# Optimization experiments

Measured on AMD Instinct MI355X. Metric: run time of the kernel, lower is better.

Reference implementation:

```python
import jax, jax.numpy as jnp
import numpy as np

D_IN, D_K, D_V = 768, 128, 768


def setup_inputs() -> dict:
    key = jax.random.key(0)
    ks = jax.random.split(key, 7)
    x = jax.random.normal(ks[0], (4, 2048, D_IN), dtype=jnp.float32)
    s_in = 1.0 / np.sqrt(D_IN)
    Wq = jax.random.uniform(ks[1], (D_IN, D_K), minval=-s_in, maxval=s_in, dtype=jnp.float32)
    bq = jax.random.uniform(ks[2], (D_K,), minval=-s_in, maxval=s_in, dtype=jnp.float32)
    Wk = jax.random.uniform(ks[3], (D_IN, D_K), minval=-s_in, maxval=s_in, dtype=jnp.float32)
    bk = jax.random.uniform(ks[4], (D_K,), minval=-s_in, maxval=s_in, dtype=jnp.float32)
    Wv = jax.random.uniform(ks[5], (D_IN, D_V), minval=-s_in, maxval=s_in, dtype=jnp.float32)
    bv = jax.random.uniform(ks[6], (D_V,), minval=-s_in, maxval=s_in, dtype=jnp.float32)
    return {"x": x, "Wq": Wq, "bq": bq, "Wk": Wk, "bk": bk, "Wv": Wv, "bv": bv}


def reference(x, Wq, bq, Wk, bk, Wv, bv):
    # q,k: [b,t,d_k]; v: [b,t,d_v]
    q = jnp.einsum('bti,ik->btk', x, Wq) + bq
    k = jnp.einsum('bti,ik->btk', x, Wk) + bk
    v = jnp.einsum('bti,iv->btv', x, Wv) + bv
    scale = 1.0 / jnp.sqrt(jnp.asarray(D_K, dtype=jnp.float32))
    scores = jnp.einsum('bqk,btk->bqt', q, k) * scale  # [b,t,t]
    attn = jax.nn.softmax(scores, axis=-1)
    return jnp.einsum('bqt,btv->bqv', attn, v)
```

## Files before the change

### kernel.cpp

```cpp
#include <hip/hip_runtime.h>
#include <stdint.h>

typedef unsigned short u16;
typedef __attribute__((ext_vector_type(8))) short short8;
typedef __attribute__((ext_vector_type(4))) float f32x4;

#define BATCH 4
#define SEQ   2048
#define DIN   768
#define DK    128
#define DV    768
#define MTOT  (BATCH*SEQ)
#define NQKV  1024

__device__ __forceinline__ u16 f2bf(float f) {
  union { float f; uint32_t u; } v; v.f = f;
  uint32_t r = v.u + 0x7FFFu + ((v.u >> 16) & 1u);
  return (u16)(r >> 16);
}
__device__ __forceinline__ float bf2f(u16 h) {
  union { uint32_t u; float f; } v; v.u = ((uint32_t)h) << 16;
  return v.f;
}

__global__ __launch_bounds__(256) void pack_all(
    const float* __restrict__ Wq, const float* __restrict__ bq,
    const float* __restrict__ Wk, const float* __restrict__ bk,
    const float* __restrict__ Wv, const float* __restrict__ bv,
    u16* __restrict__ WbT, float* __restrict__ biasP) {
  const float qs = 0.088388347648318447f;
  __shared__ u16 tile[64][72];
  int y = blockIdx.y;
  const float* W; u16* dst; int ldw, nb; float sc;
  if (y < 2)      { W = Wq; dst = WbT;                       ldw = DK; sc = qs;   nb = y;     }
  else if (y < 4) { W = Wk; dst = WbT + (size_t)DK * DIN;    ldw = DK; sc = 1.0f; nb = y - 2; }
  else            { W = Wv; dst = WbT + (size_t)2*DK * DIN;  ldw = DV; sc = 1.0f; nb = y - 4; }
  int i0 = blockIdx.x * 64;
  int n0 = nb * 64;
  int tid = threadIdx.x;
  if (blockIdx.x == 0 && y == 0) {
    for (int n = tid; n < NQKV; n += 256)
      biasP[n] = (n < DK) ? bq[n] * qs : (n < 2*DK ? bk[n - DK] : bv[n - 2*DK]);
  }
  int tr = tid >> 2;
  int tc = (tid & 3) * 16;
  const float* src = W + (size_t)(i0 + tr) * ldw + n0 + tc;
  u16 o[16];
#pragma unroll
  for (int u = 0; u < 16; u += 4) {
    float4 v = *(const float4*)(src + u);
    o[u] = f2bf(v.x * sc); o[u+1] = f2bf(v.y * sc); o[u+2] = f2bf(v.z * sc); o[u+3] = f2bf(v.w * sc);
  }
  *(uint4*)&tile[tr][tc]     = *(const uint4*)&o[0];
  *(uint4*)&tile[tr][tc + 8] = *(const uint4*)&o[8];
  __syncthreads();
  u16 tmp[16];
#pragma unroll
  for (int u = 0; u < 16; ++u) tmp[u] = tile[tc + u][tr];
  u16* d = dst + (size_t)(n0 + tr) * DIN + i0 + tc;
  *(uint4*)d       = *(const uint4*)&tmp[0];
  *(uint4*)(d + 8) = *(const uint4*)&tmp[8];
}

__global__ void convert_x(const float* __restrict__ x, u16* __restrict__ xb) {
  int i = (blockIdx.x * blockDim.x + threadIdx.x) * 4;
  float4 v = *(const float4*)(x + i);
  u16 o[4] = { f2bf(v.x), f2bf(v.y), f2bf(v.z), f2bf(v.w) };
  *(uint2*)(xb + i) = *(const uint2*)o;
}

template<int MODE, int NJ>
__global__ __launch_bounds__(512, 4) void gemm_nt(
    const u16* __restrict__ A, int lda, long long sA,
    const u16* __restrict__ BT, int ldb, long long sB,
    void* __restrict__ C0, void* __restrict__ C1, int ldc, long long sC,
    int K, int gx, int gy, const float* __restrict__ bias)
{
  __shared__ u16 As[2][128][64];
  __shared__ u16 Bs[2][NJ * 64][64];
  const int tid = threadIdx.x;
  const int l   = tid & 63;
  const int wid = tid >> 6;
  const int wm  = wid >> 2;
  const int wn  = wid & 3;

  const int nwg = gridDim.x;
  const int cpx = nwg >> 3;
  const int bid = blockIdx.x;
  const int wg  = (bid & 7) * cpx + (bid >> 3);
  const int z   = wg / (gx * gy);
  const int rem = wg - z * gx * gy;
  const int by  = rem / gx;
  const int bx  = rem - by * gx;
  const int m0  = bx * 128;
  const int n0  = by * (NJ * 64);

  A  += (size_t)z * (size_t)sA;
  BT += (size_t)z * (size_t)sB;

  f32x4 acc[4][NJ] = {};
  f32x4 accO[4] = {};
  const short8 kOnes = {16256,16256,16256,16256,16256,16256,16256,16256};

  const int lr = l >> 3;
  const int lc = ((l & 7) ^ lr) * 8;

  const int CH = 2 + NJ;
  const int ca = wid * CH;
  auto STAGE = [&](int buf, int k0) {
#pragma unroll
    for (int i = 0; i < CH; ++i) {
      int c = ca + i;
      if (c < 16) {
        const u16* src = A + (size_t)(m0 + c * 8 + lr) * lda + k0 + lc;
        __builtin_amdgcn_global_load_lds(
            (const __attribute__((address_space(1))) unsigned int*)src,
            (__attribute__((address_space(3))) unsigned int*)&As[buf][c * 8][0],
            16, 0, 0);
      } else {
        int cb = c - 16;
        const u16* src = BT + (size_t)(n0 + cb * 8 + lr) * ldb + k0 + lc;
        __builtin_amdgcn_global_load_lds(
            (const __attribute__((address_space(1))) unsigned int*)src,
            (__attribute__((address_space(3))) unsigned int*)&Bs[buf][cb * 8][0],
            16, 0, 0);
      }
    }
  };

  STAGE(0, 0);
  __syncthreads();

  int cur = 0;
  for (int k0 = 0; k0 < K; k0 += 64) {
    if (k0 + 64 < K) STAGE(cur ^ 1, k0 + 64);
#pragma unroll
    for (int ks = 0; ks < 2; ++ks) {
      short8 af[4], bg[NJ];
#pragma unroll
      for (int i = 0; i < 4; ++i) {
        int row  = wm * 64 + i * 16 + (l & 15);
        int slot = (ks * 4 + (l >> 4)) ^ (row & 7);
        af[i] = *(const short8*)&As[cur][row][slot * 8];
      }
#pragma unroll
      for (int j = 0; j < NJ; ++j) {
        int row  = wn * (NJ * 16) + j * 16 + (l & 15);
        int slot = (ks * 4 + (l >> 4)) ^ (row & 7);
        bg[j] = *(const short8*)&Bs[cur][row][slot * 8];
      }
#pragma unroll
      for (int i = 0; i < 4; ++i)
#pragma unroll
        for (int j = 0; j < NJ; ++j)
          acc[i][j] = __builtin_amdgcn_mfma_f32_16x16x32_bf16(af[i], bg[j], acc[i][j], 0, 0, 0);
      if (MODE == 0) {
#pragma unroll
        for (int i = 0; i < 4; ++i)
          accO[i] = __builtin_amdgcn_mfma_f32_16x16x32_bf16(af[i], kOnes, accO[i], 0, 0, 0);
      }
    }
    __syncthreads();
    cur ^= 1;
  }

  const int rbase = (l >> 4) * 4;
  const int cl    = l & 15;
#pragma unroll
  for (int i = 0; i < 4; ++i) {
    f32x4 rs;
    if (MODE == 0) {
#pragma unroll
      for (int q = 0; q < 4; ++q) rs[q] = 1.0f / accO[i][q];
    }
#pragma unroll
    for (int j = 0; j < NJ; ++j) {
      int col = n0 + wn * (NJ * 16) + j * 16 + cl;
      int row0 = m0 + wm * 64 + i * 16 + rbase;
      if (MODE == 0) {
#pragma unroll
        for (int q = 0; q < 4; ++q)
          ((float*)C0)[(size_t)z * (size_t)sC + (size_t)(row0 + q) * ldc + col] = acc[i][j][q] * rs[q];
      } else {
        float bv_ = bias[col];
        if (n0 < 256) {
#pragma unroll
          for (int q = 0; q < 4; ++q)
            ((u16*)C0)[(size_t)(row0 + q) * 256 + col] = f2bf(acc[i][j][q] + bv_);
        } else {
          int b = row0 >> 11, t = row0 & 2047;
          u16 o[4];
#pragma unroll
          for (int q = 0; q < 4; ++q) o[q] = f2bf(acc[i][j][q] + bv_);
          *(uint2*)&((u16*)C1)[((size_t)b * DV + (col - 256)) * SEQ + t] = *(const uint2*)o;
        }
      }
    }
  }
}

__global__ __launch_bounds__(512, 4) void sgemm_exp(
    const u16* __restrict__ qk, u16* __restrict__ P)
{
  __shared__ u16 As[128][128];
  __shared__ u16 Bs[128][128];
  const int tid = threadIdx.x;
  const int l   = tid & 63;
  const int wid = tid >> 6;
  const int wm  = wid >> 2;
  const int wn  = wid & 3;

  const int nwg = gridDim.x;
  const int cpx = nwg >> 3;
  const int bid = blockIdx.x;
  const int wg  = (bid & 7) * cpx + (bid >> 3);
  const int z   = wg >> 8;
  const int rem = wg & 255;
  const int by  = rem >> 4;
  const int bx  = rem & 15;
  const int m0  = bx * 128;
  const int n0  = by * 128;

  const u16* A  = qk + (size_t)z * SEQ * 256;
  const u16* BT = qk + DK + (size_t)z * SEQ * 256;

  const int rin  = l >> 4;
  const int s16  = l & 15;
#pragma unroll
  for (int i = 0; i < 8; ++i) {
    int c = wid * 8 + i;
    if (c < 32) {
      int r = c * 4 + rin;
      int gs = s16 ^ (r & 7);
      const u16* src = A + (size_t)(m0 + r) * 256 + gs * 8;
      __builtin_amdgcn_global_load_lds(
          (const __attribute__((address_space(1))) unsigned int*)src,
          (__attribute__((address_space(3))) unsigned int*)&As[c * 4][0],
          16, 0, 0);
    } else {
      int cb = c - 32;
      int r = cb * 4 + rin;
      int gs = s16 ^ (r & 7);
      const u16* src = BT + (size_t)(n0 + r) * 256 + gs * 8;
      __builtin_amdgcn_global_load_lds(
          (const __attribute__((address_space(1))) unsigned int*)src,
          (__attribute__((address_space(3))) unsigned int*)&Bs[cb * 4][0],
          16, 0, 0);
    }
  }
  __syncthreads();

  f32x4 acc[4][2] = {};
#pragma unroll
  for (int ks = 0; ks < 4; ++ks) {
    short8 af[4], bg[2];
#pragma unroll
    for (int i = 0; i < 4; ++i) {
      int row  = wm * 64 + i * 16 + (l & 15);
      int slot = (ks * 4 + (l >> 4)) ^ (row & 7);
      af[i] = *(const short8*)&As[row][slot * 8];
    }
#pragma unroll
    for (int j = 0; j < 2; ++j) {
      int row  = wn * 32 + j * 16 + (l & 15);
      int slot = (ks * 4 + (l >> 4)) ^ (row & 7);
      bg[j] = *(const short8*)&Bs[row][slot * 8];
    }
#pragma unroll
    for (int i = 0; i < 4; ++i)
#pragma unroll
      for (int j = 0; j < 2; ++j)
        acc[i][j] = __builtin_amdgcn_mfma_f32_16x16x32_bf16(af[i], bg[j], acc[i][j], 0, 0, 0);
  }

  const int rbase = (l >> 4) * 4;
  const int cl    = l & 15;
  u16* Pz = P + (size_t)z * SEQ * SEQ;
#pragma unroll
  for (int i = 0; i < 4; ++i)
#pragma unroll
    for (int j = 0; j < 2; ++j) {
      int col  = n0 + wn * 32 + j * 16 + cl;
      int row0 = m0 + wm * 64 + i * 16 + rbase;
#pragma unroll
      for (int q = 0; q < 4; ++q)
        Pz[(size_t)(row0 + q) * SEQ + col] = f2bf(__expf(acc[i][j][q]));
    }
}

extern "C" void kernel_launch(void* const* d_in, const int* in_sizes, int n_in,
                              void* d_out, int out_size, void* d_ws, size_t ws_size,
                              hipStream_t stream) {
  const float* x  = (const float*)d_in[0];
  const float* Wq = (const float*)d_in[1];
  const float* bq = (const float*)d_in[2];
  const float* Wk = (const float*)d_in[3];
  const float* bk = (const float*)d_in[4];
  const float* Wv = (const float*)d_in[5];
  const float* bv = (const float*)d_in[6];
  float* out = (float*)d_out;

  size_t off = 0;
  auto alloc = [&](size_t bytes) -> void* {
    void* p = (char*)d_ws + off;
    off += (bytes + 255) & ~(size_t)255;
    return p;
  };
  u16*   xb    = (u16*)alloc((size_t)MTOT * DIN * 2);
  u16*   WbT   = (u16*)alloc((size_t)NQKV * DIN * 2);
  float* biasP = (float*)alloc(NQKV * 4);
  u16*   qk    = (u16*)alloc((size_t)MTOT * 256 * 2);
  u16*   vT    = (u16*)alloc((size_t)BATCH * DV * SEQ * 2);
  u16*   P     = (u16*)alloc((size_t)BATCH * SEQ * SEQ * 2);
  if (off > ws_size) return;

  pack_all<<<dim3(DIN/64, 16), dim3(256), 0, stream>>>(Wq, bq, Wk, bk, Wv, bv, WbT, biasP);
  convert_x<<<dim3((MTOT * DIN / 4) / 256), dim3(256), 0, stream>>>(x, xb);

  gemm_nt<2, 2><<<dim3(64 * 8), dim3(512), 0, stream>>>(
      xb, DIN, 0, WbT, DIN, 0, qk, vT, 0, 0, DIN, 64, 8, biasP);

  sgemm_exp<<<dim3(16 * 16 * BATCH), dim3(512), 0, stream>>>(qk, P);

  gemm_nt<0, 3><<<dim3(16 * 4 * BATCH), dim3(512), 0, stream>>>(
      P, SEQ, (long long)SEQ * SEQ,
      vT, SEQ, (long long)DV * SEQ,
      out, nullptr, DV, (long long)SEQ * DV, SEQ, 16, 4, nullptr);
}
```

Before: 86.55 us.

## Split templated GEMM and triple-buffer P·V loads with vmcnt waits

Replaces the templated gemm_nt with two specialized kernels: a projection GEMM and a P·V GEMM. The P·V kernel keeps three LDS buffers and prefetches two tiles ahead. It waits with explicit s_waitcnt vmcnt and a raw barrier instead of __syncthreads, so global loads can stay in flight across iterations. This is meant to hide load latency in the long-K (2048) attention-output GEMM. In exchange it raises LDS use to three buffers and lowers the occupancy hint to 2, and correctness now rests on the hand-counted vmcnt values. There is no barrier between COMPUTE and the next STAGE into a different buffer, so that ordering also needs to be right.

```diff
diff --git a/kernel.cpp b/kernel.cpp
--- a/kernel.cpp
+++ b/kernel.cpp
@@ -21,6 +21,12 @@
 __device__ __forceinline__ float bf2f(u16 h) {
   union { uint32_t u; float f; } v; v.u = ((uint32_t)h) << 16;
   return v.f;
+}
+
+template<int N> __device__ __forceinline__ void wait_vmcnt() {
+  if constexpr (N == 0) asm volatile("s_waitcnt vmcnt(0)" ::: "memory");
+  else if constexpr (N == 5) asm volatile("s_waitcnt vmcnt(5)" ::: "memory");
+  else if constexpr (N == 10) asm volatile("s_waitcnt vmcnt(10)" ::: "memory");
 }
 
 __global__ __launch_bounds__(256) void pack_all(
@@ -69,15 +75,116 @@
   *(uint2*)(xb + i) = *(const uint2*)o;
 }
 
-template<int MODE, int NJ>
-__global__ __launch_bounds__(512, 4) void gemm_nt(
-    const u16* __restrict__ A, int lda, long long sA,
-    const u16* __restrict__ BT, int ldb, long long sB,
-    void* __restrict__ C0, void* __restrict__ C1, int ldc, long long sC,
-    int K, int gx, int gy, const float* __restrict__ bias)
+__global__ __launch_bounds__(512, 4) void gemm_proj(
+    const u16* __restrict__ A, const u16* __restrict__ BT,
+    u16* __restrict__ C0, u16* __restrict__ C1,
+    const float* __restrict__ bias)
 {
+  const int NJ = 2, CH = 4, gx = 64;
   __shared__ u16 As[2][128][64];
   __shared__ u16 Bs[2][NJ * 64][64];
+  const int tid = threadIdx.x;
+  const int l   = tid & 63;
+  const int wid = tid >> 6;
+  const int wm  = wid >> 2;
+  const int wn  = wid & 3;
+
+  const int nwg = gridDim.x;
+  const int cpx = nwg >> 3;
+  const int bid = blockIdx.x;
+  const int wg  = (bid & 7) * cpx + (bid >> 3);
+  const int by  = wg / gx;
+  const int bx  = wg - by * gx;
+  const int m0  = bx * 128;
+  const int n0  = by * (NJ * 64);
+
+  f32x4 acc[4][NJ] = {};
+  const int lr = l >> 3;
+  const int lc = ((l & 7) ^ lr) * 8;
+  const int ca = wid * CH;
+
+  auto STAGE = [&](int buf, int k0) {
+#pragma unroll
+    for (int i = 0; i < CH; ++i) {
+      int c = ca + i;
+      if (c < 16) {
+        const u16* src = A + (size_t)(m0 + c * 8 + lr) * DIN + k0 + lc;
+        __builtin_amdgcn_global_load_lds(
+            (const __attribute__((address_space(1))) unsigned int*)src,
+            (__attribute__((address_space(3))) unsigned int*)&As[buf][c * 8][0],
+            16, 0, 0);
+      } else {
+        int cb = c - 16;
+        const u16* src = BT + (size_t)(n0 + cb * 8 + lr) * DIN + k0 + lc;
+        __builtin_amdgcn_global_load_lds(
+            (const __attribute__((address_space(1))) unsigned int*)src,
+            (__attribute__((address_space(3))) unsigned int*)&Bs[buf][cb * 8][0],
+            16, 0, 0);
+      }
+    }
+  };
+
+  STAGE(0, 0);
+  __syncthreads();
+  int cur = 0;
+  for (int k0 = 0; k0 < DIN; k0 += 64) {
+    if (k0 + 64 < DIN) STAGE(cur ^ 1, k0 + 64);
+#pragma unroll
+    for (int ks = 0; ks < 2; ++ks) {
+      short8 af[4], bg[NJ];
+#pragma unroll
+      for (int i = 0; i < 4; ++i) {
+        int row  = wm * 64 + i * 16 + (l & 15);
+        int slot = (ks * 4 + (l >> 4)) ^ (row & 7);
+        af[i] = *(const short8*)&As[cur][row][slot * 8];
+      }
+#pragma unroll
+      for (int j = 0; j < NJ; ++j) {
+        int row  = wn * (NJ * 16) + j * 16 + (l & 15);
+        int slot = (ks * 4 + (l >> 4)) ^ (row & 7);
+        bg[j] = *(const short8*)&Bs[cur][row][slot * 8];
+      }
+#pragma unroll
+      for (int i = 0; i < 4; ++i)
+#pragma unroll
+        for (int j = 0; j < NJ; ++j)
+          acc[i][j] = __builtin_amdgcn_mfma_f32_16x16x32_bf16(af[i], bg[j], acc[i][j], 0, 0, 0);
+    }
+    __syncthreads();
+    cur ^= 1;
+  }
+
+  const int rbase = (l >> 4) * 4;
+  const int cl    = l & 15;
+#pragma unroll
+  for (int i = 0; i < 4; ++i) {
+#pragma unroll
+    for (int j = 0; j < NJ; ++j) {
+      int col = n0 + wn * (NJ * 16) + j * 16 + cl;
+      int row0 = m0 + wm * 64 + i * 16 + rbase;
+      float bv_ = bias[col];
+      if (n0 < 256) {
+#pragma unroll
+        for (int q = 0; q < 4; ++q)
+          C0[(size_t)(row0 + q) * 256 + col] = f2bf(acc[i][j][q] + bv_);
+      } else {
+        int b = row0 >> 11, t = row0 & 2047;
+        u16 o[4];
+#pragma unroll
+        for (int q = 0; q < 4; ++q) o[q] = f2bf(acc[i][j][q] + bv_);
+        *(uint2*)&C1[((size_t)b * DV + (col - 256)) * SEQ + t] = *(const uint2*)o;
+      }
+    }
+  }
+}
+
+__global__ __launch_bounds__(512, 2) void gemm_pv(
+    const u16* __restrict__ P, const u16* __restrict__ vT,
+    float* __restrict__ out)
+{
+  const int NJ = 3, CH = 5, gx = 16, gy = 4, NT = SEQ / 64;
+  __shared__ u16 As[3][128][64];
+  __shared__ u16 Bs[3][NJ * 64][64];
   const int tid = threadIdx.x;
   const int l   = tid & 63;
   const int wid = tid >> 6;
@@ -95,8 +202,8 @@
   const int m0  = bx * 128;
   const int n0  = by * (NJ * 64);
 
-  A  += (size_t)z * (size_t)sA;
-  BT += (size_t)z * (size_t)sB;
+  const u16* A  = P  + (size_t)z * SEQ * SEQ;
+  const u16* BT = vT + (size_t)z * DV * SEQ;
 
   f32x4 acc[4][NJ] = {};
   f32x4 accO[4] = {};
@@ -104,22 +211,21 @@
 
   const int lr = l >> 3;
   const int lc = ((l & 7) ^ lr) * 8;
-
-  const int CH = 2 + NJ;
   const int ca = wid * CH;
+
   auto STAGE = [&](int buf, int k0) {
 #pragma unroll
     for (int i = 0; i < CH; ++i) {
       int c = ca + i;
       if (c < 16) {
-        const u16* src = A + (size_t)(m0 + c * 8 + lr) * lda + k0 + lc;
+        const u16* src = A + (size_t)(m0 + c * 8 + lr) * SEQ + k0 + lc;
         __builtin_amdgcn_global_load_lds(
             (const __attribute__((address_space(1))) unsigned int*)src,
             (__attribute__((address_space(3))) unsigned int*)&As[buf][c * 8][0],
             16, 0, 0);
       } else {
         int cb = c - 16;
-        const u16* src = BT + (size_t)(n0 + cb * 8 + lr) * ldb + k0 + lc;
+        const u16* src = BT + (size_t)(n0 + cb * 8 + lr) * SEQ + k0 + lc;
         __builtin_amdgcn_global_load_lds(
             (const __attribute__((address_space(1))) unsigned int*)src,
             (__attribute__((address_space(3))) unsigned int*)&Bs[buf][cb * 8][0],
@@ -128,12 +234,7 @@
     }
   };
 
-  STAGE(0, 0);
-  __syncthreads();
-
-  int cur = 0;
-  for (int k0 = 0; k0 < K; k0 += 64) {
-    if (k0 + 64 < K) STAGE(cur ^ 1, k0 + 64);
+  auto COMPUTE = [&](int buf) {
 #pragma unroll
     for (int ks = 0; ks < 2; ++ks) {
       short8 af[4], bg[NJ];
@@ -141,60 +242,53 @@
       for (int i = 0; i < 4; ++i) {
         int row  = wm * 64 + i * 16 + (l & 15);
         int slot = (ks * 4 + (l >> 4)) ^ (row & 7);
-        af[i] = *(const short8*)&As[cur][row][slot * 8];
+        af[i] = *(const short8*)&As[buf][row][slot * 8];
       }
 #pragma unroll
       for (int j = 0; j < NJ; ++j) {
         int row  = wn * (NJ * 16) + j * 16 + (l & 15);
         int slot = (ks * 4 + (l >> 4)) ^ (row & 7);
-        bg[j] = *(const short8*)&Bs[cur][row][slot * 8];
+        bg[j] = *(const short8*)&Bs[buf][row][slot * 8];
       }
 #pragma unroll
       for (int i = 0; i < 4; ++i)
 #pragma unroll
         for (int j = 0; j < NJ; ++j)
           acc[i][j] = __builtin_amdgcn_mfma_f32_16x16x32_bf16(af[i], bg[j], acc[i][j], 0, 0, 0);
-      if (MODE == 0) {
-#pragma unroll
-        for (int i = 0; i < 4; ++i)
-          accO[i] = __builtin_amdgcn_mfma_f32_16x16x32_bf16(af[i], kOnes, accO[i], 0, 0, 0);
-      }
-    }
-    __syncthreads();
-    cur ^= 1;
-  }
+#pragma unroll
+      for (int i = 0; i < 4; ++i)
+        accO[i] = __builtin_amdgcn_mfma_f32_16x16x32_bf16(af[i], kOnes, accO[i], 0, 0, 0);
+    }
+  };
+
+  STAGE(0, 0);
+  STAGE(1, 64);
+  int cur = 0;
+  for (int t = 0; t < NT - 1; ++t) {
+    wait_vmcnt<CH>();
+    __builtin_amdgcn_s_barrier();
+    COMPUTE(cur);
+    if (t + 2 < NT) STAGE(cur + 2 >= 3 ? cur - 1 : cur + 2, (t + 2) * 64);
+    cur = (cur + 1 == 3) ? 0 : cur + 1;
+  }
+  wait_vmcnt<0>();
+  __builtin_amdgcn_s_barrier();
+  COMPUTE(cur);
 
   const int rbase = (l >> 4) * 4;
   const int cl    = l & 15;
 #pragma unroll
   for (int i = 0; i < 4; ++i) {
     f32x4 rs;
-    if (MODE == 0) {
-#pragma unroll
-      for (int q = 0; q < 4; ++q) rs[q] = 1.0f / accO[i][q];
-    }
+#pragma unroll
+    for (int q = 0; q < 4; ++q) rs[q] = 1.0f / accO[i][q];
 #pragma unroll
     for (int j = 0; j < NJ; ++j) {
-      int col = n0 + wn * (NJ * 16) + j * 16 + cl;
+      int col  = n0 + wn * (NJ * 16) + j * 16 + cl;
       int row0 = m0 + wm * 64 + i * 16 + rbase;
-      if (MODE == 0) {
-#pragma unroll
-        for (int q = 0; q < 4; ++q)
-          ((float*)C0)[(size_t)z * (size_t)sC + (size_t)(row0 + q) * ldc + col] = acc[i][j][q] * rs[q];
-      } else {
-        float bv_ = bias[col];
-        if (n0 < 256) {
-#pragma unroll
-          for (int q = 0; q < 4; ++q)
-            ((u16*)C0)[(size_t)(row0 + q) * 256 + col] = f2bf(acc[i][j][q] + bv_);
-        } else {
-          int b = row0 >> 11, t = row0 & 2047;
-          u16 o[4];
-#pragma unroll
-          for (int q = 0; q < 4; ++q) o[q] = f2bf(acc[i][j][q] + bv_);
-          *(uint2*)&((u16*)C1)[((size_t)b * DV + (col - 256)) * SEQ + t] = *(const uint2*)o;
-        }
-      }
+#pragma unroll
+      for (int q = 0; q < 4; ++q)
+        out[(size_t)z * SEQ * DV + (size_t)(row0 + q) * DV + col] = acc[i][j][q] * rs[q];
     }
   }
 }
@@ -317,13 +411,9 @@
   pack_all<<<dim3(DIN/64, 16), dim3(256), 0, stream>>>(Wq, bq, Wk, bk, Wv, bv, WbT, biasP);
   convert_x<<<dim3((MTOT * DIN / 4) / 256), dim3(256), 0, stream>>>(x, xb);
 
-  gemm_nt<2, 2><<<dim3(64 * 8), dim3(512), 0, stream>>>(
-      xb, DIN, 0, WbT, DIN, 0, qk, vT, 0, 0, DIN, 64, 8, biasP);
+  gemm_proj<<<dim3(64 * 8), dim3(512), 0, stream>>>(xb, WbT, qk, vT, biasP);
 
   sgemm_exp<<<dim3(16 * 16 * BATCH), dim3(512), 0, stream>>>(qk, P);
 
-  gemm_nt<0, 3><<<dim3(16 * 4 * BATCH), dim3(512), 0, stream>>>(
-      P, SEQ, (long long)SEQ * SEQ,
-      vT, SEQ, (long long)DV * SEQ,
-      out, nullptr, DV, (long long)SEQ * DV, SEQ, 16, 4, nullptr);
-}
+  gemm_pv<<<dim3(16 * 4 * BATCH), dim3(512), 0, stream>>>(P, vT, out);
+}
```

New measurement: 85.52 us. Within noise of the previous version (-1.2%).
